# Kernel optimization log

Hardware: AMD Instinct MI355X
Metric: run time of the kernel (lower is better)

## Reference

```python
import jax, jax.numpy as jnp
import numpy as np
from functools import partial

M, K, N = 256, 32, 2048
TOL = 1e-6


def _masked_solve(AtA, Atb, P):
    # Solve (A^T A)[P,P] z_P = (A^T b)[P], zeros elsewhere, via a masked k x k system.
    Pm = P.astype(AtA.dtype)
    Msys = AtA * (Pm[:, None] * Pm[None, :]) + jnp.diag(1.0 - Pm)
    z = jnp.linalg.solve(Msys, Atb * Pm)
    return z * Pm


def _nnls_col(AtA, Atb):
    # fnnls active-set NNLS for one column: argmin_{s>=0} ||x - A s||^2
    k = Atb.shape[0]
    max_it = 3 * k

    def inner_cond(st):
        P, s, z, it = st
        return jnp.logical_and(jnp.any(jnp.logical_and(P, z <= TOL)), it < max_it)

    def inner_body(st):
        P, s, z, it = st
        mask = jnp.logical_and(P, z <= TOL)
        denom = s - z
        ratio = jnp.where(mask, s / jnp.where(denom != 0, denom, 1.0), jnp.inf)
        alpha = jnp.min(ratio)
        s = s + alpha * (z - s)
        P = jnp.logical_and(P, s > TOL)
        s = jnp.where(P, s, 0.0)
        z = _masked_solve(AtA, Atb, P)
        return (P, s, z, it + 1)

    def outer_cond(st):
        P, s, it = st
        w = Atb - AtA @ s
        return jnp.logical_and(jnp.any(jnp.logical_and(~P, w > TOL)), it < max_it)

    def outer_body(st):
        P, s, it = st
        w = jnp.where(P, -jnp.inf, Atb - AtA @ s)
        j = jnp.argmax(w)
        P = P.at[j].set(True)
        z = _masked_solve(AtA, Atb, P)
        P, s, z, _ = jax.lax.while_loop(inner_cond, inner_body, (P, s, z, jnp.int32(0)))
        s = jnp.where(P, z, 0.0)
        return (P, s, it + 1)

    P0 = jnp.zeros(k, dtype=bool)
    s0 = jnp.zeros(k, dtype=Atb.dtype)
    _, s, _ = jax.lax.while_loop(outer_cond, outer_body, (P0, s0, jnp.int32(0)))
    return s


def setup_inputs() -> dict:
    key = jax.random.key(0)
    kx, ka = jax.random.split(key)
    X = jax.random.uniform(kx, (M, N), dtype=jnp.float32)  # nonneg data matrix
    A = jnp.abs(jax.random.normal(ka, (M, K), dtype=jnp.float32))  # module's A init
    return {"input": X, "A": A}


def reference(input, A):
    # S = q(X, A): column-wise nonneg least squares, batched over the n columns.
    AtA = A.T @ A            # [k,k]
    AtX = A.T @ input        # [k,n]
    S = jax.vmap(_nnls_col, in_axes=(None, 1), out_axes=1)(AtA, AtX)  # [k,n]
    return S
```

## Files before the change

kernel.cpp:

```cpp
#include <hip/hip_runtime.h>
#include <math.h>

#define KDIM 32
#define MDIM 256
#define NDIM 2048
#define W_TOL 1e-3f

__device__ __forceinline__ float lane_bcast(float x, int lane) {
  return __int_as_float(__builtin_amdgcn_readlane(__float_as_int(x), lane));
}
__device__ __forceinline__ float rcp_newton(float x) {
  float r;
  asm("v_rcp_f32 %0, %1" : "=v"(r) : "v"(x));
  r = r * (2.0f - x * r);
  return r;
}
__device__ __forceinline__ float rcp_fast(float x) {
  float r;
  asm("v_rcp_f32 %0, %1" : "=v"(r) : "v"(x));
  return r;
}

__global__ __launch_bounds__(1024) void ata_partial(const float* __restrict__ A,
                                                    float* __restrict__ part) {
  __shared__ float As[32 * KDIM];
  const int t = threadIdx.x, g = blockIdx.x;
  As[t] = A[g * 32 * KDIM + t];
  __syncthreads();
  const int i = t >> 5, j = t & 31;
  float acc = 0.f;
#pragma unroll
  for (int mm = 0; mm < 32; ++mm)
    acc = fmaf(As[mm * KDIM + i], As[mm * KDIM + j], acc);
  part[g * 1024 + t] = acc;
}

__global__ __launch_bounds__(64) void inv_kernel(const float* __restrict__ part,
                                                 float* __restrict__ AtA,
                                                 float* __restrict__ Ainv) {
  __shared__ float AtAs[KDIM * 33];
  const int l = threadIdx.x;
  const int r = l & 31;
#pragma unroll
  for (int q4 = 0; q4 < 4; ++q4) {
    const int f4 = q4 * 64 + l;
    float4 s = {0.f, 0.f, 0.f, 0.f};
#pragma unroll
    for (int g = 0; g < 8; ++g) {
      const float4 v = reinterpret_cast<const float4*>(part)[g * 256 + f4];
      s.x += v.x; s.y += v.y; s.z += v.z; s.w += v.w;
    }
    reinterpret_cast<float4*>(AtA)[f4] = s;
    const int e = f4 * 4, row = e >> 5, col = e & 31;
    AtAs[row * 33 + col + 0] = s.x;
    AtAs[row * 33 + col + 1] = s.y;
    AtAs[row * 33 + col + 2] = s.z;
    AtAs[row * 33 + col + 3] = s.w;
  }
  __syncthreads();
  float m[KDIM], g[KDIM];
#pragma unroll
  for (int c = 0; c < KDIM; ++c) {
    m[c] = AtAs[r * 33 + c];
    g[c] = (r == c) ? 1.f : 0.f;
  }
  float myinv = 0.f;
#pragma unroll
  for (int j = 0; j < KDIM; ++j) {
    const float inv = rcp_newton(lane_bcast(m[j], j));
    const float f = (r != j) ? m[j] * inv : 0.f;
#pragma unroll
    for (int c = j + 1; c < KDIM; ++c) m[c] = fmaf(-f, lane_bcast(m[c], j), m[c]);
#pragma unroll
    for (int c = 0; c < KDIM; ++c) g[c] = fmaf(-f, lane_bcast(g[c], j), g[c]);
    if (r == j) myinv = inv;
  }
  if (l < 32) {
#pragma unroll
    for (int c = 0; c < KDIM; ++c) Ainv[r * KDIM + c] = myinv * g[c];
  }
}

__global__ __launch_bounds__(64, 2) void nnls_kernel(const float* __restrict__ A,
                                                     const float* __restrict__ AtA_g,
                                                     const float* __restrict__ Ainv_g,
                                                     const float* __restrict__ X,
                                                     float* __restrict__ S) {
  const int l = threadIdx.x;
  const int r = l & 31;
  const int n = blockIdx.x;

  float x4[4];
#pragma unroll
  for (int q = 0; q < 4; ++q) x4[q] = X[(q * 64 + l) * NDIM + n];
  float cur[KDIM];
#pragma unroll
  for (int k = 0; k < KDIM; ++k) cur[k] = 0.f;
#pragma unroll
  for (int q = 0; q < 4; ++q) {
    const int m = q * 64 + l;
#pragma unroll
    for (int qq = 0; qq < 8; ++qq) {
      const float4 a4 = reinterpret_cast<const float4*>(A + m * KDIM)[qq];
      cur[4 * qq + 0] = fmaf(a4.x, x4[q], cur[4 * qq + 0]);
      cur[4 * qq + 1] = fmaf(a4.y, x4[q], cur[4 * qq + 1]);
      cur[4 * qq + 2] = fmaf(a4.z, x4[q], cur[4 * qq + 2]);
      cur[4 * qq + 3] = fmaf(a4.w, x4[q], cur[4 * qq + 3]);
    }
  }
#pragma unroll
  for (int k = 0; k < KDIM; ++k) cur[k] += __shfl_xor(cur[k], 32);
#pragma unroll
  for (int o = 16; o >= 1; o >>= 1) {
#pragma unroll
    for (int i = 0; i < o; ++i) {
      const bool hi = (l & o) != 0;
      const float a = cur[i], b = cur[i + o];
      const float mine = hi ? b : a;
      const float send = hi ? a : b;
      cur[i] = mine + __shfl_xor(send, o);
    }
  }
  const float atb = cur[0];

  float ata[KDIM], g[KDIM];
#pragma unroll
  for (int q = 0; q < KDIM / 4; ++q) {
    const float4 v = reinterpret_cast<const float4*>(AtA_g + r * KDIM)[q];
    ata[4 * q + 0] = v.x; ata[4 * q + 1] = v.y; ata[4 * q + 2] = v.z; ata[4 * q + 3] = v.w;
    const float4 u = reinterpret_cast<const float4*>(Ainv_g + r * KDIM)[q];
    g[4 * q + 0] = u.x; g[4 * q + 1] = u.y; g[4 * q + 2] = u.z; g[4 * q + 3] = u.w;
  }

  float y;
  {
    float s0 = 0.f, s1 = 0.f, s2 = 0.f, s3 = 0.f;
#pragma unroll
    for (int c = 0; c < KDIM; c += 4) {
      s0 = fmaf(g[c + 0], lane_bcast(atb, c + 0), s0);
      s1 = fmaf(g[c + 1], lane_bcast(atb, c + 1), s1);
      s2 = fmaf(g[c + 2], lane_bcast(atb, c + 2), s2);
      s3 = fmaf(g[c + 3], lane_bcast(atb, c + 3), s3);
    }
    y = (s0 + s1) + (s2 + s3);
  }

  auto solve_dual = [&](unsigned int Pm) -> float {
    const unsigned int Rm = ~Pm;
    const int p = __popc(Pm);
    if (p <= 32 - p) {
      const bool actl = (Pm >> r) & 1u;
      float m[KDIM];
#pragma unroll
      for (int c = 0; c < KDIM; ++c)
        m[c] = (actl && ((Pm >> c) & 1u)) ? ata[c] : ((r == c) ? 1.f : 0.f);
      float rhs = actl ? atb : 0.f;
      float myinv = 0.f;
#pragma unroll
      for (int j = 0; j < KDIM; ++j) {
        if ((Pm >> j) & 1u) {
          const float inv = rcp_fast(lane_bcast(m[j], j));
          const float f = (r != j) ? m[j] * inv : 0.f;
#pragma unroll
          for (int c = j + 1; c < KDIM; ++c) m[c] = fmaf(-f, lane_bcast(m[c], j), m[c]);
          rhs = fmaf(-f, lane_bcast(rhs, j), rhs);
          if (r == j) myinv = inv;
        }
      }
      return rhs * myinv;
    } else {
      const bool reml = (Rm >> r) & 1u;
      float m[KDIM];
#pragma unroll
      for (int c = 0; c < KDIM; ++c)
        m[c] = (reml && ((Rm >> c) & 1u)) ? g[c] : ((r == c) ? 1.f : 0.f);
      float rhs = reml ? y : 0.f;
      float myinv = 0.f;
#pragma unroll
      for (int j = 0; j < KDIM; ++j) {
        if ((Rm >> j) & 1u) {
          const float inv = rcp_fast(lane_bcast(m[j], j));
          const float f = (r != j) ? m[j] * inv : 0.f;
#pragma unroll
          for (int c = j + 1; c < KDIM; ++c) m[c] = fmaf(-f, lane_bcast(m[c], j), m[c]);
          rhs = fmaf(-f, lane_bcast(rhs, j), rhs);
          if (r == j) myinv = inv;
        }
      }
      const float u = rhs * myinv;
      float z0 = y, z1 = 0.f, z2 = 0.f, z3 = 0.f;
#pragma unroll
      for (int c = 0; c < KDIM; c += 4) {
        z0 = fmaf(-g[c + 0], lane_bcast(u, c + 0), z0);
        z1 = fmaf(-g[c + 1], lane_bcast(u, c + 1), z1);
        z2 = fmaf(-g[c + 2], lane_bcast(u, c + 2), z2);
        z3 = fmaf(-g[c + 3], lane_bcast(u, c + 3), z3);
      }
      return (z0 + z1) + (z2 + z3);
    }
  };

  unsigned int P = (unsigned int)(__ballot(atb > 1e-6f) & 0xffffffffull);
  float z = (P == 0xffffffffu) ? y : solve_dual(P);

  float zeps = 0.f, weps = W_TOL;
  int best = 1000;
  bool conv = false;
  for (int it = 0; it < 8; ++it) {
    const bool act = (P >> r) & 1u;
    float s0 = 0.f, s1 = 0.f, s2 = 0.f, s3 = 0.f;
#pragma unroll
    for (int c = 0; c < KDIM; c += 4) {
      s0 = fmaf(ata[c + 0], lane_bcast(z, c + 0), s0);
      s1 = fmaf(ata[c + 1], lane_bcast(z, c + 1), s1);
      s2 = fmaf(ata[c + 2], lane_bcast(z, c + 2), s2);
      s3 = fmaf(ata[c + 3], lane_bcast(z, c + 3), s3);
    }
    const float w = atb - ((s0 + s1) + (s2 + s3));
    const bool pred = act ? (z < -zeps) : (w > weps);
    const unsigned int u = (unsigned int)(__ballot(pred) & 0xffffffffull);
    if (u == 0u) { conv = true; break; }
    const int ninf = __popc(u);
    if (ninf < best) {
      best = ninf;
    } else {
      zeps = fminf(zeps * 4.f + 2e-6f, 2.5e-4f);
      weps *= 4.f;
    }
    P = (P & ~(u & P)) | (u & ~P);
    z = solve_dual(P);
  }

  if (!conv) {
    const unsigned int drop =
        (unsigned int)(__ballot(((P >> r) & 1u) && (z < -2.5e-4f)) & 0xffffffffull);
    if (drop != 0u) {
      P &= ~drop;
      z = solve_dual(P);
    }
  }

  if (l < KDIM) S[r * NDIM + n] = ((P >> r) & 1u) ? fmaxf(z, 0.f) : 0.f;
}

extern "C" void kernel_launch(void* const* d_in, const int* in_sizes, int n_in,
                              void* d_out, int out_size, void* d_ws, size_t ws_size,
                              hipStream_t stream) {
  const float* X = (const float*)d_in[0];
  const float* A = (const float*)d_in[1];
  float* S = (float*)d_out;
  float* AtA = (float*)d_ws;
  float* Ainv = AtA + KDIM * KDIM;
  float* part = Ainv + KDIM * KDIM;

  ata_partial<<<8, 1024, 0, stream>>>(A, part);
  inv_kernel<<<1, 64, 0, stream>>>(part, AtA, Ainv);
  nnls_kernel<<<NDIM, 64, 0, stream>>>(A, AtA, Ainv, X, S);
}
```

Baseline: 40.76 us.

## Merge AtA/inverse prep with batched AtX computation into one prep kernel

```diff
diff --git a/kernel.cpp b/kernel.cpp
--- a/kernel.cpp
+++ b/kernel.cpp
@@ -21,107 +21,113 @@
   return r;
 }
 
-__global__ __launch_bounds__(1024) void ata_partial(const float* __restrict__ A,
-                                                    float* __restrict__ part) {
-  __shared__ float As[32 * KDIM];
-  const int t = threadIdx.x, g = blockIdx.x;
-  As[t] = A[g * 32 * KDIM + t];
+__global__ __launch_bounds__(256) void prep_kernel(const float* __restrict__ A,
+                                                   const float* __restrict__ X,
+                                                   float* __restrict__ AtA,
+                                                   float* __restrict__ Ainv,
+                                                   float* __restrict__ AtXt) {
+  __shared__ float buf[8448];
+  const int t = threadIdx.x;
+  {
+    const float4* A4 = reinterpret_cast<const float4*>(A);
+    float4* B4 = reinterpret_cast<float4*>(buf);
+#pragma unroll
+    for (int i = 0; i < 8; ++i) B4[t + 256 * i] = A4[t + 256 * i];
+  }
   __syncthreads();
-  const int i = t >> 5, j = t & 31;
-  float acc = 0.f;
-#pragma unroll
-  for (int mm = 0; mm < 32; ++mm)
-    acc = fmaf(As[mm * KDIM + i], As[mm * KDIM + j], acc);
-  part[g * 1024 + t] = acc;
-}
-
-__global__ __launch_bounds__(64) void inv_kernel(const float* __restrict__ part,
-                                                 float* __restrict__ AtA,
-                                                 float* __restrict__ Ainv) {
-  __shared__ float AtAs[KDIM * 33];
-  const int l = threadIdx.x;
-  const int r = l & 31;
-#pragma unroll
-  for (int q4 = 0; q4 < 4; ++q4) {
-    const int f4 = q4 * 64 + l;
-    float4 s = {0.f, 0.f, 0.f, 0.f};
-#pragma unroll
-    for (int g = 0; g < 8; ++g) {
-      const float4 v = reinterpret_cast<const float4*>(part)[g * 256 + f4];
-      s.x += v.x; s.y += v.y; s.z += v.z; s.w += v.w;
-    }
-    reinterpret_cast<float4*>(AtA)[f4] = s;
-    const int e = f4 * 4, row = e >> 5, col = e & 31;
-    AtAs[row * 33 + col + 0] = s.x;
-    AtAs[row * 33 + col + 1] = s.y;
-    AtAs[row * 33 + col + 2] = s.z;
-    AtAs[row * 33 + col + 3] = s.w;
-  }
-  __syncthreads();
-  float m[KDIM], g[KDIM];
-#pragma unroll
-  for (int c = 0; c < KDIM; ++c) {
-    m[c] = AtAs[r * 33 + c];
-    g[c] = (r == c) ? 1.f : 0.f;
-  }
-  float myinv = 0.f;
-#pragma unroll
-  for (int j = 0; j < KDIM; ++j) {
-    const float inv = rcp_newton(lane_bcast(m[j], j));
-    const float f = (r != j) ? m[j] * inv : 0.f;
-#pragma unroll
-    for (int c = j + 1; c < KDIM; ++c) m[c] = fmaf(-f, lane_bcast(m[c], j), m[c]);
-#pragma unroll
-    for (int c = 0; c < KDIM; ++c) g[c] = fmaf(-f, lane_bcast(g[c], j), g[c]);
-    if (r == j) myinv = inv;
-  }
-  if (l < 32) {
-#pragma unroll
-    for (int c = 0; c < KDIM; ++c) Ainv[r * KDIM + c] = myinv * g[c];
-  }
-}
-
-__global__ __launch_bounds__(64, 2) void nnls_kernel(const float* __restrict__ A,
-                                                     const float* __restrict__ AtA_g,
+
+  if (blockIdx.x < 64) {
+    const int nl = t & 31;
+    const int ch = t >> 5;
+    const int n = blockIdx.x * 32 + nl;
+    float acc[KDIM];
+#pragma unroll
+    for (int k = 0; k < KDIM; ++k) acc[k] = 0.f;
+#pragma unroll 4
+    for (int mm = 0; mm < 32; ++mm) {
+      const int m = ch * 32 + mm;
+      const float x = X[m * NDIM + n];
+#pragma unroll
+      for (int qq = 0; qq < 8; ++qq) {
+        const float4 a4 = *reinterpret_cast<const float4*>(&buf[m * KDIM + qq * 4]);
+        acc[4 * qq + 0] = fmaf(a4.x, x, acc[4 * qq + 0]);
+        acc[4 * qq + 1] = fmaf(a4.y, x, acc[4 * qq + 1]);
+        acc[4 * qq + 2] = fmaf(a4.z, x, acc[4 * qq + 2]);
+        acc[4 * qq + 3] = fmaf(a4.w, x, acc[4 * qq + 3]);
+      }
+    }
+    __syncthreads();
+#pragma unroll
+    for (int k = 0; k < KDIM; ++k) buf[ch * 1056 + nl * 33 + k] = acc[k];
+    __syncthreads();
+    float v[4];
+#pragma unroll
+    for (int q = 0; q < 4; ++q) {
+      const int f = t * 4 + q, kk = f & 31, nn = f >> 5;
+      float s = 0.f;
+#pragma unroll
+      for (int g = 0; g < 8; ++g) s += buf[g * 1056 + nn * 33 + kk];
+      v[q] = s;
+    }
+    const float4 o = {v[0], v[1], v[2], v[3]};
+    reinterpret_cast<float4*>(AtXt + blockIdx.x * 32 * KDIM)[t] = o;
+  } else {
+    const int i = t >> 3, j0 = (t & 7) * 4;
+    float a0 = 0.f, a1 = 0.f, a2 = 0.f, a3 = 0.f;
+    for (int m = 0; m < MDIM; ++m) {
+      const float ai = buf[m * KDIM + i];
+      const float4 vj = *reinterpret_cast<const float4*>(&buf[m * KDIM + j0]);
+      a0 = fmaf(ai, vj.x, a0);
+      a1 = fmaf(ai, vj.y, a1);
+      a2 = fmaf(ai, vj.z, a2);
+      a3 = fmaf(ai, vj.w, a3);
+    }
+    __syncthreads();
+    {
+      const float4 o = {a0, a1, a2, a3};
+      reinterpret_cast<float4*>(AtA)[t] = o;
+    }
+    buf[i * 33 + j0 + 0] = a0;
+    buf[i * 33 + j0 + 1] = a1;
+    buf[i * 33 + j0 + 2] = a2;
+    buf[i * 33 + j0 + 3] = a3;
+    __syncthreads();
+    if (t < 64) {
+      const int r = t & 31;
+      float m_[KDIM], g_[KDIM];
+#pragma unroll
+      for (int c = 0; c < KDIM; ++c) {
+        m_[c] = buf[r * 33 + c];
+        g_[c] = (r == c) ? 1.f : 0.f;
+      }
+      float myinv = 0.f;
+#pragma unroll
+      for (int j = 0; j < KDIM; ++j) {
+        const float inv = rcp_newton(lane_bcast(m_[j], j));
+        const float f = (r != j) ? m_[j] * inv : 0.f;
+#pragma unroll
+        for (int c = j + 1; c < KDIM; ++c) m_[c] = fmaf(-f, lane_bcast(m_[c], j), m_[c]);
+#pragma unroll
+        for (int c = 0; c < KDIM; ++c) g_[c] = fmaf(-f, lane_bcast(g_[c], j), g_[c]);
+        if (r == j) myinv = inv;
+      }
+      if (t < 32) {
+#pragma unroll
+        for (int c = 0; c < KDIM; ++c) Ainv[r * KDIM + c] = myinv * g_[c];
+      }
+    }
+  }
+}
+
+__global__ __launch_bounds__(64, 2) void nnls_kernel(const float* __restrict__ AtA_g,
                                                      const float* __restrict__ Ainv_g,
-                                                     const float* __restrict__ X,
+                                                     const float* __restrict__ AtXt,
                                                      float* __restrict__ S) {
   const int l = threadIdx.x;
   const int r = l & 31;
   const int n = blockIdx.x;
 
-  float x4[4];
-#pragma unroll
-  for (int q = 0; q < 4; ++q) x4[q] = X[(q * 64 + l) * NDIM + n];
-  float cur[KDIM];
-#pragma unroll
-  for (int k = 0; k < KDIM; ++k) cur[k] = 0.f;
-#pragma unroll
-  for (int q = 0; q < 4; ++q) {
-    const int m = q * 64 + l;
-#pragma unroll
-    for (int qq = 0; qq < 8; ++qq) {
-      const float4 a4 = reinterpret_cast<const float4*>(A + m * KDIM)[qq];
-      cur[4 * qq + 0] = fmaf(a4.x, x4[q], cur[4 * qq + 0]);
-      cur[4 * qq + 1] = fmaf(a4.y, x4[q], cur[4 * qq + 1]);
-      cur[4 * qq + 2] = fmaf(a4.z, x4[q], cur[4 * qq + 2]);
-      cur[4 * qq + 3] = fmaf(a4.w, x4[q], cur[4 * qq + 3]);
-    }
-  }
-#pragma unroll
-  for (int k = 0; k < KDIM; ++k) cur[k] += __shfl_xor(cur[k], 32);
-#pragma unroll
-  for (int o = 16; o >= 1; o >>= 1) {
-#pragma unroll
-    for (int i = 0; i < o; ++i) {
-      const bool hi = (l & o) != 0;
-      const float a = cur[i], b = cur[i + o];
-      const float mine = hi ? b : a;
-      const float send = hi ? a : b;
-      cur[i] = mine + __shfl_xor(send, o);
-    }
-  }
-  const float atb = cur[0];
+  const float atb = AtXt[n * KDIM + r];
 
   float ata[KDIM], g[KDIM];
 #pragma unroll
@@ -251,9 +257,8 @@
   float* S = (float*)d_out;
   float* AtA = (float*)d_ws;
   float* Ainv = AtA + KDIM * KDIM;
-  float* part = Ainv + KDIM * KDIM;
-
-  ata_partial<<<8, 1024, 0, stream>>>(A, part);
-  inv_kernel<<<1, 64, 0, stream>>>(part, AtA, Ainv);
-  nnls_kernel<<<NDIM, 64, 0, stream>>>(A, AtA, Ainv, X, S);
-}
+  float* AtXt = Ainv + KDIM * KDIM;
+
+  prep_kernel<<<65, 256, 0, stream>>>(A, X, AtA, Ainv, AtXt);
+  nnls_kernel<<<NDIM, 64, 0, stream>>>(AtA, Ainv, AtXt, S);
+}
```

Result: faster. 32.65 us, median of 3 (-19.9%).
